# Optimization experiments

Hardware: AMD Instinct MI355X
Metric: run time of the kernel (lower is better)

Reference implementation:

```python
import jax, jax.numpy as jnp
import numpy as np

N_MODULES = 32
POINTER_DIM = 64
CONTENT_DIM = 256
N_CYCLES = 1
EPS = 1e-42  # denormal but representable in float32, as in original


def setup_inputs() -> dict:
    key = jax.random.key(0)
    ks = jax.random.split(key, 8)
    B, T, M, P, C = 16, 128, N_MODULES, POINTER_DIM, CONTENT_DIM
    pointers = jax.random.normal(ks[0], (B, T, P), dtype=jnp.float32)
    contents = jax.random.normal(ks[1], (B, T, C), dtype=jnp.float32)
    # learned parameters (kaiming-uniform-like scaling)
    receivers = jax.random.uniform(ks[2], (M, P), minval=-1.0, maxval=1.0) / np.sqrt(P)
    memories = jax.random.uniform(ks[3], (M, C, C), minval=-1.0, maxval=1.0) / np.sqrt(C)
    # per-module routing MLP: Linear(C+P -> P), ReLU, Linear(P -> P), ReLU
    W1 = jax.random.uniform(ks[4], (M, C + P, P), minval=-1.0, maxval=1.0) / np.sqrt(C + P)
    b1 = jnp.zeros((M, P), dtype=jnp.float32)
    W2 = jax.random.uniform(ks[5], (M, P, P), minval=-1.0, maxval=1.0) / np.sqrt(P)
    b2 = jnp.zeros((M, P), dtype=jnp.float32)
    return {"pointers": pointers, "contents": contents, "receivers": receivers,
            "memories": memories, "W1": W1, "b1": b1, "W2": W2, "b2": b2}


def _cycle(pointers, contents, mems, receivers, W1, b1, W2, b2):
    # in-weightings: relu(tanh(receivers @ pointers^T)) -> [B, M, T]
    w_in = jax.nn.relu(jnp.tanh(jnp.einsum('mp,btp->bmt', receivers, pointers)))
    # weighted gather-reduce over tokens
    eff_c = jnp.einsum('bmt,btc->bmc', w_in, contents)   # [B, M, C]
    eff_p = jnp.einsum('bmt,btp->bmp', w_in, pointers)   # [B, M, P]
    # memory read: batched matvec
    out_c = jnp.einsum('bmcd,bmd->bmc', mems, eff_c)     # [B, M, C]
    # per-module routing MLP (batched over modules with einsum)
    routing_in = jnp.concatenate([eff_p, eff_c], axis=-1)            # [B, M, P+C]
    h = jax.nn.relu(jnp.einsum('bmi,mio->bmo', routing_in, W1) + b1)  # [B, M, P]
    out_p = jax.nn.relu(jnp.einsum('bmi,mio->bmo', h, W2) + b2)       # [B, M, P]
    # out-weightings over modules
    w_out = jax.nn.relu(jnp.tanh(jnp.einsum('bmp,bnp->bmn', out_p, out_p)))  # [B, M, M]
    eff_out_c = jnp.einsum('bmn,bnc->bmc', w_out, out_c)  # [B, M, C]
    # outer-product memory update
    normed_in = eff_c / (jnp.sum(eff_c * eff_c, axis=-1, keepdims=True) + EPS)
    perfect = jnp.einsum('bmc,bmd->bmcd', eff_out_c, normed_in)  # [B, M, C, C]
    mems = 0.5 * (mems + perfect)
    return out_p, out_c, mems


def reference(pointers, contents, receivers, memories, W1, b1, W2, b2):
    B = pointers.shape[0]
    mems = jnp.broadcast_to(memories[None], (B,) + memories.shape)
    for _ in range(N_CYCLES):
        pointers, contents, mems = _cycle(pointers, contents, mems,
                                          receivers, W1, b1, W2, b2)
    return pointers, contents, mems
```

## Files before the change

### kernel.cpp

```cpp
#include <hip/hip_runtime.h>
#include <math.h>

#define BB 16
#define TT 128
#define MM 32
#define PP 64
#define CC 256

typedef float f32x4 __attribute__((ext_vector_type(4)));

__global__ __launch_bounds__(512) void K1_front(
        const float* __restrict__ pointers,
        const float* __restrict__ contents,
        const float* __restrict__ receivers,
        const float* __restrict__ memories,
        const float* __restrict__ W1,
        const float* __restrict__ b1,
        const float* __restrict__ W2,
        const float* __restrict__ b2,
        float* __restrict__ eff_c_ws,
        float* __restrict__ outp_g,
        float* __restrict__ outc_g) {
    const int bm = blockIdx.x;
    const int b = bm >> 5, m = bm & 31;
    const int tid = threadIdx.x;
    const int lane = tid & 63, w = tid >> 6;

    __shared__ float w_in[TT];
    __shared__ float ri[PP + CC];
    __shared__ float partc[2][CC];
    __shared__ float part8[8][PP];
    __shared__ float h[PP];
    __shared__ float outc_s[CC];

    {
        const int t = tid >> 2, q = tid & 3;
        const float4* pr4 = reinterpret_cast<const float4*>(pointers + (b * TT + t) * PP + q * 16);
        const float4* rc4 = reinterpret_cast<const float4*>(receivers + m * PP + q * 16);
        float s = 0.f;
        #pragma unroll
        for (int k = 0; k < 4; ++k) {
            float4 v = pr4[k], rv = rc4[k];
            s += v.x * rv.x + v.y * rv.y + v.z * rv.z + v.w * rv.w;
        }
        s += __shfl_xor(s, 1, 64);
        s += __shfl_xor(s, 2, 64);
        if (q == 0) {
            float th = tanhf(s);
            w_in[t] = th > 0.f ? th : 0.f;
        }
    }
    __syncthreads();
    {
        const int c = tid & 255, g = tid >> 8;
        const float* cb = contents + (b * TT + g * 64) * CC + c;
        float acc = 0.f;
        #pragma unroll 4
        for (int t = 0; t < 64; ++t) acc += w_in[g * 64 + t] * cb[t * CC];
        partc[g][c] = acc;
    }
    {
        const int p = tid & 63, g = tid >> 6;
        const float* pb = pointers + (b * TT + g * 16) * PP + p;
        float acc = 0.f;
        #pragma unroll
        for (int t = 0; t < 16; ++t) acc += w_in[g * 16 + t] * pb[t * PP];
        part8[g][p] = acc;
    }
    __syncthreads();
    if (tid < CC) {
        float e = partc[0][tid] + partc[1][tid];
        ri[PP + tid] = e;
        eff_c_ws[bm * CC + tid] = e;
    } else if (tid < CC + PP) {
        const int p = tid - CC;
        float a = 0.f;
        #pragma unroll
        for (int g = 0; g < 8; ++g) a += part8[g][p];
        ri[p] = a;
    }
    __syncthreads();

    {
        const int g = lane >> 4, j = lane & 15;
        float4 e_reg[4];
        #pragma unroll
        for (int k = 0; k < 4; ++k)
            e_reg[k] = *reinterpret_cast<const float4*>(&ri[PP + 4 * (j + 16 * k)]);
        const float4* mem4 = reinterpret_cast<const float4*>(memories) + m * (CC * CC / 4);
        #pragma unroll
        for (int i = 0; i < 8; ++i) {
            const int c = w * 32 + i * 4 + g;
            const float4* row4 = mem4 + c * 64;
            float s = 0.f;
            #pragma unroll
            for (int k = 0; k < 4; ++k) {
                float4 mv = row4[j + 16 * k];
                s += mv.x * e_reg[k].x + mv.y * e_reg[k].y
                   + mv.z * e_reg[k].z + mv.w * e_reg[k].w;
            }
            s += __shfl_xor(s, 1, 64);
            s += __shfl_xor(s, 2, 64);
            s += __shfl_xor(s, 4, 64);
            s += __shfl_xor(s, 8, 64);
            if (j == 0) outc_s[c] = s;
        }
    }

    {
        const float* w1 = W1 + m * 320 * 64;
        float acc = 0.f;
        const int i0 = w * 40;
        #pragma unroll 8
        for (int i = i0; i < i0 + 40; ++i) acc += ri[i] * w1[i * 64 + lane];
        __syncthreads();
        part8[w][lane] = acc;
    }
    __syncthreads();
    if (tid < PP) {
        float s = b1[m * PP + tid];
        #pragma unroll
        for (int g = 0; g < 8; ++g) s += part8[g][tid];
        h[tid] = s > 0.f ? s : 0.f;
    }
    __syncthreads();
    {
        const float* w2 = W2 + m * 64 * 64;
        float acc = 0.f;
        const int i0 = w * 8;
        #pragma unroll
        for (int i = i0; i < i0 + 8; ++i) acc += h[i] * w2[i * 64 + lane];
        part8[w][lane] = acc;
    }
    __syncthreads();
    if (tid < PP) {
        float s = b2[m * PP + tid];
        #pragma unroll
        for (int g = 0; g < 8; ++g) s += part8[g][tid];
        outp_g[bm * PP + tid] = s > 0.f ? s : 0.f;
    }
    if (tid < CC) outc_g[bm * CC + tid] = outc_s[tid];
}

__global__ __launch_bounds__(256) void K3_fused(
        const float* __restrict__ memories,
        const float* __restrict__ outp_g,
        const float* __restrict__ outc_g,
        const float* __restrict__ eff_c_ws,
        float* __restrict__ mems_out) {
    const int gid = blockIdx.x;
    const int b = gid >> 8;
    const int m = (gid >> 3) & 31, cs = gid & 7;
    const int bm = b * MM + m;
    const int tid = threadIdx.x;
    const int lane = tid & 63, w = tid >> 6;

    __shared__ float wout_s[MM];
    __shared__ float nrm_s[CC];
    __shared__ float eoc_s[32];
    __shared__ float red[4];

    const float ec = eff_c_ws[bm * CC + tid];
    {
        float v = ec * ec;
        #pragma unroll
        for (int off = 32; off; off >>= 1) v += __shfl_xor(v, off, 64);
        if (lane == 0) red[w] = v;
    }
    {
        const int n = tid >> 3, j = tid & 7;
        const float* opm = outp_g + bm * PP + j * 8;
        const float* opn = outp_g + (b * MM + n) * PP + j * 8;
        float s = 0.f;
        #pragma unroll
        for (int k = 0; k < 8; ++k) s += opm[k] * opn[k];
        s += __shfl_xor(s, 1, 64);
        s += __shfl_xor(s, 2, 64);
        s += __shfl_xor(s, 4, 64);
        if (j == 0) {
            float th = tanhf(s);
            wout_s[n] = th > 0.f ? th : 0.f;
        }
    }
    __syncthreads();
    nrm_s[tid] = ec / (red[0] + red[1] + red[2] + red[3] + 1e-42f);
    {
        const int c_local = tid >> 3, k = tid & 7;
        const int c = cs * 32 + c_local;
        const float* cb = outc_g + b * MM * CC + c;
        float s = 0.f;
        #pragma unroll
        for (int kk = 0; kk < 4; ++kk)
            s += wout_s[k * 4 + kk] * cb[(k * 4 + kk) * CC];
        s += __shfl_xor(s, 1, 64);
        s += __shfl_xor(s, 2, 64);
        s += __shfl_xor(s, 4, 64);
        if (k == 0) eoc_s[c_local] = s;
    }
    __syncthreads();

    const float4 nv = reinterpret_cast<const float4*>(nrm_s)[lane];
    const f32x4* mem4 = reinterpret_cast<const f32x4*>(memories) + (m * CC + cs * 32) * 64;
    f32x4* out4 = reinterpret_cast<f32x4*>(mems_out) + (bm * CC + cs * 32) * 64;

    #pragma unroll
    for (int it = 0; it < 8; ++it) {
        const int idx = it * 256 + tid;
        const float e = eoc_s[it * 4 + w];
        f32x4 mv = mem4[idx];
        f32x4 o;
        o.x = 0.5f * (mv.x + e * nv.x);
        o.y = 0.5f * (mv.y + e * nv.y);
        o.z = 0.5f * (mv.z + e * nv.z);
        o.w = 0.5f * (mv.w + e * nv.w);
        __builtin_nontemporal_store(o, &out4[idx]);
    }
}

extern "C" void kernel_launch(void* const* d_in, const int* in_sizes, int n_in,
                              void* d_out, int out_size, void* d_ws, size_t ws_size,
                              hipStream_t stream) {
    const float* pointers  = (const float*)d_in[0];
    const float* contents  = (const float*)d_in[1];
    const float* receivers = (const float*)d_in[2];
    const float* memories  = (const float*)d_in[3];
    const float* W1 = (const float*)d_in[4];
    const float* b1 = (const float*)d_in[5];
    const float* W2 = (const float*)d_in[6];
    const float* b2 = (const float*)d_in[7];

    float* out      = (float*)d_out;
    float* outp_g   = out;
    float* outc_g   = out + 32768;
    float* mems_out = out + 32768 + 131072;

    float* eff_c = (float*)d_ws;

    hipLaunchKernelGGL(K1_front, dim3(BB * MM), dim3(512), 0, stream,
                       pointers, contents, receivers, memories, W1, b1, W2, b2,
                       eff_c, outp_g, outc_g);
    hipLaunchKernelGGL(K3_fused, dim3(BB * MM * 8), dim3(256), 0, stream,
                       memories, outp_g, outc_g, eff_c, mems_out);
}
```

Before: 46.80 us.

## Fuse front and memory-update kernels into one cooperative kernel with grid sync

```diff
diff --git a/kernel.cpp b/kernel.cpp
--- a/kernel.cpp
+++ b/kernel.cpp
@@ -1,5 +1,8 @@
 #include <hip/hip_runtime.h>
+#include <hip/hip_cooperative_groups.h>
 #include <math.h>
+
+namespace cg = cooperative_groups;
 
 #define BB 16
 #define TT 128
@@ -9,7 +12,7 @@
 
 typedef float f32x4 __attribute__((ext_vector_type(4)));
 
-__global__ __launch_bounds__(512) void K1_front(
+__global__ __launch_bounds__(512, 4) void KF_all(
         const float* __restrict__ pointers,
         const float* __restrict__ contents,
         const float* __restrict__ receivers,
@@ -18,20 +21,24 @@
         const float* __restrict__ b1,
         const float* __restrict__ W2,
         const float* __restrict__ b2,
-        float* __restrict__ eff_c_ws,
         float* __restrict__ outp_g,
-        float* __restrict__ outc_g) {
+        float* __restrict__ outc_g,
+        float* __restrict__ mems_out) {
     const int bm = blockIdx.x;
     const int b = bm >> 5, m = bm & 31;
     const int tid = threadIdx.x;
     const int lane = tid & 63, w = tid >> 6;
 
     __shared__ float w_in[TT];
-    __shared__ float ri[PP + CC];
+    __shared__ __align__(16) float ri[PP + CC];
     __shared__ float partc[2][CC];
     __shared__ float part8[8][PP];
     __shared__ float h[PP];
     __shared__ float outc_s[CC];
+    __shared__ float wout_s[MM];
+    __shared__ __align__(16) float nrm_s[CC];
+    __shared__ float eoc_s[CC];
+    __shared__ float red[4];
 
     {
         const int t = tid >> 2, q = tid & 3;
@@ -69,9 +76,7 @@
     }
     __syncthreads();
     if (tid < CC) {
-        float e = partc[0][tid] + partc[1][tid];
-        ri[PP + tid] = e;
-        eff_c_ws[bm * CC + tid] = e;
+        ri[PP + tid] = partc[0][tid] + partc[1][tid];
     } else if (tid < CC + PP) {
         const int p = tid - CC;
         float a = 0.f;
@@ -140,73 +145,55 @@
         outp_g[bm * PP + tid] = s > 0.f ? s : 0.f;
     }
     if (tid < CC) outc_g[bm * CC + tid] = outc_s[tid];
-}
-
-__global__ __launch_bounds__(256) void K3_fused(
-        const float* __restrict__ memories,
-        const float* __restrict__ outp_g,
-        const float* __restrict__ outc_g,
-        const float* __restrict__ eff_c_ws,
-        float* __restrict__ mems_out) {
-    const int gid = blockIdx.x;
-    const int b = gid >> 8;
-    const int m = (gid >> 3) & 31, cs = gid & 7;
-    const int bm = b * MM + m;
-    const int tid = threadIdx.x;
-    const int lane = tid & 63, w = tid >> 6;
-
-    __shared__ float wout_s[MM];
-    __shared__ float nrm_s[CC];
-    __shared__ float eoc_s[32];
-    __shared__ float red[4];
-
-    const float ec = eff_c_ws[bm * CC + tid];
-    {
+
+    cg::this_grid().sync();
+
+    float ec = 0.f;
+    if (tid < CC) {
+        ec = ri[PP + tid];
         float v = ec * ec;
         #pragma unroll
         for (int off = 32; off; off >>= 1) v += __shfl_xor(v, off, 64);
         if (lane == 0) red[w] = v;
     }
     {
-        const int n = tid >> 3, j = tid & 7;
-        const float* opm = outp_g + bm * PP + j * 8;
-        const float* opn = outp_g + (b * MM + n) * PP + j * 8;
-        float s = 0.f;
-        #pragma unroll
-        for (int k = 0; k < 8; ++k) s += opm[k] * opn[k];
+        const int n = tid >> 4, j = tid & 15;
+        const float4 a  = *reinterpret_cast<const float4*>(outp_g + bm * PP + j * 4);
+        const float4 c4 = *reinterpret_cast<const float4*>(outp_g + (b * MM + n) * PP + j * 4);
+        float s = a.x * c4.x + a.y * c4.y + a.z * c4.z + a.w * c4.w;
         s += __shfl_xor(s, 1, 64);
         s += __shfl_xor(s, 2, 64);
         s += __shfl_xor(s, 4, 64);
+        s += __shfl_xor(s, 8, 64);
         if (j == 0) {
             float th = tanhf(s);
             wout_s[n] = th > 0.f ? th : 0.f;
         }
     }
     __syncthreads();
-    nrm_s[tid] = ec / (red[0] + red[1] + red[2] + red[3] + 1e-42f);
-    {
-        const int c_local = tid >> 3, k = tid & 7;
-        const int c = cs * 32 + c_local;
-        const float* cb = outc_g + b * MM * CC + c;
-        float s = 0.f;
-        #pragma unroll
-        for (int kk = 0; kk < 4; ++kk)
-            s += wout_s[k * 4 + kk] * cb[(k * 4 + kk) * CC];
-        s += __shfl_xor(s, 1, 64);
-        s += __shfl_xor(s, 2, 64);
-        s += __shfl_xor(s, 4, 64);
-        if (k == 0) eoc_s[c_local] = s;
-    }
+    if (tid < CC) {
+        const float ss = red[0] + red[1] + red[2] + red[3];
+        nrm_s[tid] = ec / (ss + 1e-42f);
+    }
+    {
+        const int g = tid >> 8, c = tid & 255;
+        const float* cb = outc_g + (b * MM + g * 16) * CC + c;
+        float acc = 0.f;
+        #pragma unroll
+        for (int k = 0; k < 16; ++k) acc += wout_s[g * 16 + k] * cb[k * CC];
+        partc[g][c] = acc;
+    }
+    __syncthreads();
+    if (tid < CC) eoc_s[tid] = partc[0][tid] + partc[1][tid];
     __syncthreads();
 
     const float4 nv = reinterpret_cast<const float4*>(nrm_s)[lane];
-    const f32x4* mem4 = reinterpret_cast<const f32x4*>(memories) + (m * CC + cs * 32) * 64;
-    f32x4* out4 = reinterpret_cast<f32x4*>(mems_out) + (bm * CC + cs * 32) * 64;
-
-    #pragma unroll
-    for (int it = 0; it < 8; ++it) {
-        const int idx = it * 256 + tid;
-        const float e = eoc_s[it * 4 + w];
+    const f32x4* mem4 = reinterpret_cast<const f32x4*>(memories) + m * (CC * CC / 4);
+    f32x4* out4 = reinterpret_cast<f32x4*>(mems_out) + bm * (CC * CC / 4);
+    #pragma unroll 8
+    for (int it = 0; it < 32; ++it) {
+        const int idx = it * 512 + tid;
+        const float e = eoc_s[it * 8 + w];
         f32x4 mv = mem4[idx];
         f32x4 o;
         o.x = 0.5f * (mv.x + e * nv.x);
@@ -234,11 +221,11 @@
     float* outc_g   = out + 32768;
     float* mems_out = out + 32768 + 131072;
 
-    float* eff_c = (float*)d_ws;
-
-    hipLaunchKernelGGL(K1_front, dim3(BB * MM), dim3(512), 0, stream,
-                       pointers, contents, receivers, memories, W1, b1, W2, b2,
-                       eff_c, outp_g, outc_g);
-    hipLaunchKernelGGL(K3_fused, dim3(BB * MM * 8), dim3(256), 0, stream,
-                       memories, outp_g, outc_g, eff_c, mems_out);
+    void* args[] = {
+        (void*)&pointers, (void*)&contents, (void*)&receivers, (void*)&memories,
+        (void*)&W1, (void*)&b1, (void*)&W2, (void*)&b2,
+        (void*)&outp_g, (void*)&outc_g, (void*)&mems_out
+    };
+    hipLaunchCooperativeKernel((const void*)KF_all, dim3(BB * MM), dim3(512),
+                               args, 0, stream);
 }
```

Result: slower. 100.5 us (+114.9%).
